# Optimization experiments

Hardware: AMD Instinct MI355X
Metric: run time of the kernel (lower is better)

Reference implementation:

```python
import jax, jax.numpy as jnp
import numpy as np

SLOPE = 0.01  # nn.LeakyReLU(negative_slope=0.01)
B, D, H, E, NH = 16384, 17, 256, 64, 4  # batch, input_dim, hidden, embed, heads

def lrelu(x):
    return jnp.where(x >= 0, x, SLOPE * x)

def setup_inputs() -> dict:
    key = jax.random.key(0)
    ks = jax.random.split(key, 16)
    s = 0.08  # ~xavier-ish scale for these widths
    return {
        "x":   jax.random.normal(ks[0], (B, D), jnp.float32),
        # per-dimension subnets, batched over the D=17 subnet axis
        "W1":  jax.random.normal(ks[1], (D, H), jnp.float32) * 1.0,      # 1 -> H
        "b1":  jnp.zeros((D, H), jnp.float32),
        "Wm":  jax.random.normal(ks[2], (2, D, H, H), jnp.float32) * s,  # two middle H->H layers
        "bm":  jnp.zeros((2, D, H), jnp.float32),
        "Wf":  jax.random.normal(ks[3], (D, H, E), jnp.float32) * s,     # H -> output_dim(=E)
        "bf":  jnp.zeros((D, E), jnp.float32),
        # MultiheadAttention in/out projections (torch Linear convention: y = x @ W.T + b)
        "Wq":  jax.random.normal(ks[4], (E, E), jnp.float32) * s,
        "bq":  jnp.zeros((E,), jnp.float32),
        "Wk":  jax.random.normal(ks[5], (E, E), jnp.float32) * s,
        "bk":  jnp.zeros((E,), jnp.float32),
        "Wv":  jax.random.normal(ks[6], (E, E), jnp.float32) * s,
        "bv":  jnp.zeros((E,), jnp.float32),
        "Wo":  jax.random.normal(ks[7], (E, E), jnp.float32) * s,
        "bo":  jnp.zeros((E,), jnp.float32),
        "Wfc": jax.random.normal(ks[8], (E, 1), jnp.float32) * s,
        "bfc": jnp.zeros((1,), jnp.float32),
    }

def reference(x, W1, b1, Wm, bm, Wf, bf, Wq, bq, Wk, bk, Wv, bv, Wo, bo, Wfc, bfc):
    b, d = x.shape
    # batched tiny subnets: first layer is (B,D,1) x (D,1,H) == outer product
    h = lrelu(x[:, :, None] * W1[None] + b1)                    # (B,D,H)
    for l in range(Wm.shape[0]):                                 # fixed 2 middle layers
        h = lrelu(jnp.einsum('bih,iho->bio', h, Wm[l]) + bm[l])  # (B,D,H)
    tokens = jnp.einsum('bih,iho->bio', h, Wf) + bf              # (B,D,E); proj is None (dims match)
    # self-attention (torch MultiheadAttention, batch_first)
    hd = E // NH
    def heads(t):
        return t.reshape(b, d, NH, hd).transpose(0, 2, 1, 3)     # (B,NH,D,hd)
    q = heads(tokens @ Wq.T + bq)
    k = heads(tokens @ Wk.T + bk)
    v = heads(tokens @ Wv.T + bv)
    scores = jnp.einsum('bhqd,bhkd->bhqk', q, k) / jnp.sqrt(jnp.asarray(hd, x.dtype))
    attn = jax.nn.softmax(scores, axis=-1)                       # (B,NH,D,D)
    o = jnp.einsum('bhqk,bhkd->bhqd', attn, v)
    o = o.transpose(0, 2, 1, 3).reshape(b, d, E) @ Wo.T + bo     # (B,D,E)
    pooled = o.mean(axis=1)                                      # (B,E)
    return lrelu(pooled @ Wfc + bfc)                             # (B,1)
```

## Files before the change

kernel.cpp:

```cpp
#include <hip/hip_runtime.h>
#include <hip/hip_bf16.h>

#define B_N   16384
#define D_N   17
#define H_N   256
#define E_N   64

typedef __attribute__((ext_vector_type(8))) short bf16x8;
typedef __attribute__((ext_vector_type(4))) float f32x4;

#define WAITV(N) asm volatile("s_waitcnt vmcnt(" #N ")" ::: "memory")
#define WAITL()  asm volatile("s_waitcnt lgkmcnt(0)" ::: "memory")
#define BAR()    __builtin_amdgcn_s_barrier()

static __device__ __forceinline__ short f2bf(float f){
  unsigned u = __builtin_bit_cast(unsigned, f);
  unsigned r = (u + 0x7fffu + ((u >> 16) & 1u)) >> 16;
  return (short)(unsigned short)r;
}
static __device__ __forceinline__ float bf2f(short s){
  unsigned u = ((unsigned)(unsigned short)s) << 16;
  return __builtin_bit_cast(float, u);
}
static __device__ __forceinline__ float lrelu(float v){ return fmaxf(v, 0.01f * v); }

static __device__ __forceinline__ void gload_lds16(const short* g, short* l){
  __builtin_amdgcn_global_load_lds(
      (const __attribute__((address_space(1))) unsigned int*)g,
      (__attribute__((address_space(3))) unsigned int*)l, 16, 0, 0);
}

__global__ void transpose_convert(const float* __restrict__ in, short* __restrict__ outp,
                                  int R, int C){
  __shared__ float tile[32][33];
  int g = blockIdx.z;
  const float* inp = in + (size_t)g * R * C;
  short* op = outp + (size_t)g * R * C;
  int c0 = blockIdx.x * 32, r0 = blockIdx.y * 32;
  for (int i = threadIdx.y; i < 32; i += 8)
    tile[i][threadIdx.x] = inp[(size_t)(r0 + i) * C + c0 + threadIdx.x];
  __syncthreads();
  for (int i = threadIdx.y; i < 32; i += 8)
    op[(size_t)(c0 + i) * R + r0 + threadIdx.x] = f2bf(tile[threadIdx.x][i]);
}

__global__ void convert_wqkv(const float* __restrict__ Wq, const float* __restrict__ Wk,
                             const float* __restrict__ Wv, short* __restrict__ outw){
  int i = blockIdx.x * 256 + threadIdx.x;
  int g = i >> 12, r = i & 4095;
  const float* W = (g == 0) ? Wq : (g == 1 ? Wk : Wv);
  outw[i] = f2bf(W[r]);
}

__global__ void wcomb_kernel(const float* __restrict__ Wo, const float* __restrict__ Wfc,
                             const float* __restrict__ bo, const float* __restrict__ bfc,
                             float* __restrict__ wcomb){
  int e = threadIdx.x;
  float acc = 0.f;
  for (int eo = 0; eo < 64; ++eo) acc += Wo[eo * 64 + e] * Wfc[eo];
  wcomb[e] = acc;
  if (e == 0){
    float bc = bfc[0];
    for (int eo = 0; eo < 64; ++eo) bc += bo[eo] * Wfc[eo];
    wcomb[64] = bc;
  }
}

static __device__ __forceinline__ void stage_w256(const short* Wt, int kk, short* wb,
                                                  int tid, int wave){
  #pragma unroll
  for (int r = 0; r < 2; ++r){
    int li = r * 512 + tid;
    int n  = li >> 2;
    int cc = (li & 3) ^ ((n >> 1) & 3);
    gload_lds16(Wt + n * 256 + kk * 32 + cc * 8,
                wb + (size_t)(r * 512 + wave * 64) * 8);
  }
}
static __device__ __forceinline__ void stage_wf_pair(const short* Wfd, int kk0, short* wb,
                                                     int tid, int wave){
  int sub = tid >> 8;
  int u   = tid & 255;
  int n   = u >> 2;
  int cc  = (u & 3) ^ ((n >> 1) & 3);
  gload_lds16(Wfd + n * 256 + (kk0 + sub) * 32 + cc * 8,
              wb + sub * 2048 + (size_t)((wave & 3) * 64) * 8);
}

__global__ __launch_bounds__(512, 2) void subnet_kernel(
    const float* __restrict__ x, const float* __restrict__ W1, const float* __restrict__ b1,
    const float* __restrict__ bm, const float* __restrict__ bf_,
    const float* __restrict__ bq, const float* __restrict__ bk, const float* __restrict__ bv,
    const short* __restrict__ WmT, const short* __restrict__ WfT, const short* __restrict__ Wqkv,
    short* __restrict__ qkv)
{
  __shared__ short hbuf[2][64 * 256];
  __shared__ short wbuf[3][256 * 32];

  int wg = blockIdx.x;
  int idx = (wg & 7) * 272 + (wg >> 3);
  const int d  = idx >> 7;
  const int m0 = (idx & 127) * 128;

  const int tid = threadIdx.x;
  const int lane = tid & 63, wave = tid >> 6;
  const int mh = wave >> 2, wv = wave & 3;
  const int l15 = lane & 15, lhi = lane >> 4;
  short* hb = &hbuf[mh][0];

  const short* WtL0 = WmT + (size_t)(0 * D_N + d) * (H_N * H_N);
  const short* WtL1 = WmT + (size_t)(1 * D_N + d) * (H_N * H_N);
  const short* Wfd  = WfT + (size_t)d * (E_N * H_N);

  stage_w256(WtL0, 0, &wbuf[0][0], tid, wave);
  stage_w256(WtL0, 1, &wbuf[1][0], tid, wave);

  {
    const int kp = tid & 127;
    const int mq = tid >> 7;
    const int tl = mq >> 1, half = mq & 1;
    short* hp = &hbuf[tl][0];
    const float w1a = W1[d * H_N + 2 * kp], w1b = W1[d * H_N + 2 * kp + 1];
    const float b1a = b1[d * H_N + 2 * kp], b1b = b1[d * H_N + 2 * kp + 1];
    #pragma unroll
    for (int i = 0; i < 32; ++i){
      int m = half * 32 + i;
      float xv = x[(size_t)(m0 + tl * 64 + m) * D_N + d];
      unsigned lo = (unsigned short)f2bf(lrelu(xv * w1a + b1a));
      unsigned hi = (unsigned short)f2bf(lrelu(xv * w1b + b1b));
      int byte = m * 512 + ((((kp >> 2) ^ (m & 7))) << 4) + ((kp & 3) << 2);
      *(unsigned*)((char*)hp + byte) = lo | (hi << 16);
    }
  }
  WAITL();

  for (int L = 0; L < 2; ++L){
    const float* bias = bm + (size_t)(L * D_N + d) * H_N;
    f32x4 acc[4][4];
    #pragma unroll
    for (int a = 0; a < 4; ++a)
      #pragma unroll
      for (int c = 0; c < 4; ++c) acc[a][c] = (f32x4){0.f, 0.f, 0.f, 0.f};

    for (int kk = 0; kk < 8; ++kk){
      const int s = L * 8 + kk;
      if (s == 15) { WAITV(1); } else { WAITV(2); }
      BAR();
      const int s2 = s + 2;
      if (s2 < 8)       stage_w256(WtL0, s2,            &wbuf[s2 % 3][0], tid, wave);
      else if (s2 < 16) stage_w256(WtL1, s2 - 8,        &wbuf[s2 % 3][0], tid, wave);
      else              stage_wf_pair(Wfd, (s2 - 16) * 2, &wbuf[s2 % 3][0], tid, wave);

      const short* wb = &wbuf[s % 3][0];
      bf16x8 af[4], bfr[4];
      #pragma unroll
      for (int fr = 0; fr < 4; ++fr){
        int row = fr * 16 + l15;
        int cch = kk * 4 + lhi;
        af[fr] = *(const bf16x8*)((const char*)hb + row * 512 + ((cch ^ (row & 7)) << 4));
      }
      #pragma unroll
      for (int fc = 0; fc < 4; ++fc){
        int n = wv * 64 + fc * 16 + l15;
        bfr[fc] = *(const bf16x8*)((const char*)wb + n * 64 + ((lhi ^ ((n >> 1) & 3)) << 4));
      }
      #pragma unroll
      for (int fr = 0; fr < 4; ++fr)
        #pragma unroll
        for (int fc = 0; fc < 4; ++fc)
          acc[fr][fc] = __builtin_amdgcn_mfma_f32_16x16x32_bf16(af[fr], bfr[fc], acc[fr][fc], 0, 0, 0);
    }
    BAR();
    #pragma unroll
    for (int fr = 0; fr < 4; ++fr)
      #pragma unroll
      for (int fc = 0; fc < 4; ++fc)
        #pragma unroll
        for (int j = 0; j < 4; ++j){
          int row = fr * 16 + lhi * 4 + j;
          int col = wv * 64 + fc * 16 + l15;
          float v = lrelu(acc[fr][fc][j] + bias[col]);
          int byte = row * 512 + ((((col >> 3) ^ (row & 7))) << 4) + ((col & 7) << 1);
          *(short*)((char*)hb + byte) = f2bf(v);
        }
    WAITL();
  }

  {
    const int r0 = wv * 16;
    f32x4 acc[4];
    #pragma unroll
    for (int fc = 0; fc < 4; ++fc) acc[fc] = (f32x4){0.f, 0.f, 0.f, 0.f};
    for (int t = 0; t < 4; ++t){
      if (t == 3) { WAITV(0); } else { WAITV(1); }
      BAR();
      if (t < 2) stage_wf_pair(Wfd, (t + 2) * 2, &wbuf[(18 + t) % 3][0], tid, wave);
      const short* wbase = &wbuf[(16 + t) % 3][0];
      #pragma unroll
      for (int kkh = 0; kkh < 2; ++kkh){
        int kk = 2 * t + kkh;
        int row = r0 + l15;
        int cch = kk * 4 + lhi;
        bf16x8 a = *(const bf16x8*)((const char*)hb + row * 512 + ((cch ^ (row & 7)) << 4));
        const short* wbs = wbase + kkh * 2048;
        #pragma unroll
        for (int fc = 0; fc < 4; ++fc){
          int n = fc * 16 + l15;
          bf16x8 b = *(const bf16x8*)((const char*)wbs + n * 64 + ((lhi ^ ((n >> 1) & 3)) << 4));
          acc[fc] = __builtin_amdgcn_mfma_f32_16x16x32_bf16(a, b, acc[fc], 0, 0, 0);
        }
      }
    }
    BAR();
    #pragma unroll
    for (int fc = 0; fc < 4; ++fc)
      #pragma unroll
      for (int j = 0; j < 4; ++j){
        int row = r0 + lhi * 4 + j;
        int col = fc * 16 + l15;
        float v = acc[fc][j] + bf_[d * E_N + col];
        int byte = row * 128 + ((((col >> 3) ^ (row & 7))) << 4) + ((col & 7) << 1);
        *(short*)((char*)hb + byte) = f2bf(v);
      }
    WAITL();
    BAR();
  }

  {
    f32x4 acc[4][3];
    #pragma unroll
    for (int fr = 0; fr < 4; ++fr)
      #pragma unroll
      for (int fc = 0; fc < 3; ++fc) acc[fr][fc] = (f32x4){0.f, 0.f, 0.f, 0.f};
    #pragma unroll
    for (int kk = 0; kk < 2; ++kk){
      bf16x8 af[4];
      #pragma unroll
      for (int fr = 0; fr < 4; ++fr){
        int row = fr * 16 + l15;
        int cch = kk * 4 + lhi;
        af[fr] = *(const bf16x8*)((const char*)hb + row * 128 + ((cch ^ (row & 7)) << 4));
      }
      bf16x8 bb[3];
      #pragma unroll
      for (int fc = 0; fc < 3; ++fc){
        int n = wv * 48 + fc * 16 + l15;
        bb[fc] = *(const bf16x8*)(Wqkv + (size_t)n * E_N + kk * 32 + lhi * 8);
      }
      #pragma unroll
      for (int fr = 0; fr < 4; ++fr)
        #pragma unroll
        for (int fc = 0; fc < 3; ++fc)
          acc[fr][fc] = __builtin_amdgcn_mfma_f32_16x16x32_bf16(af[fr], bb[fc], acc[fr][fc], 0, 0, 0);
    }
    #pragma unroll
    for (int fr = 0; fr < 4; ++fr)
      #pragma unroll
      for (int fc = 0; fc < 3; ++fc)
        #pragma unroll
        for (int j = 0; j < 4; ++j){
          int n = wv * 48 + fc * 16 + l15;
          int g = n >> 6, nl = n & 63;
          float bias = (g == 0) ? bq[nl] : (g == 1 ? bk[nl] : bv[nl]);
          int bg = m0 + mh * 64 + fr * 16 + lhi * 4 + j;
          float v = acc[fr][fc][j] + bias;
          qkv[((size_t)bg * D_N + d) * 192 + n] = f2bf(v);
        }
  }
}

__global__ __launch_bounds__(256, 2) void attn_kernel(
    const short* __restrict__ qkv, const float* __restrict__ wc, float* __restrict__ out)
{
  __shared__ short smem[4][17 * 192];
  const int tid = threadIdx.x, lane = tid & 63, wave = tid >> 6;
  const int h = lane >> 4, iq = lane & 15;

  const int b = blockIdx.x * 4 + wave;
  const short* src = qkv + (size_t)b * (17 * 192);
  for (int g0 = lane; g0 < 408; g0 += 64){
    int i = g0 / 24, c = g0 % 24;
    bf16x8 v = *(const bf16x8*)(src + g0 * 8);
    *(bf16x8*)((char*)&smem[wave][0] + i * 384 + ((c ^ (i & 7)) << 4)) = v;
  }

  float vt = 0.f, vt16 = 0.f;
  #pragma unroll
  for (int u2 = 0; u2 < 2; ++u2){
    int cch = 16 + 2 * h + u2;
    bf16x8 vj  = *(const bf16x8*)((char*)&smem[wave][0] + iq * 384 + ((cch ^ (iq & 7)) << 4));
    bf16x8 v16 = *(const bf16x8*)((char*)&smem[wave][0] + 16 * 384 + (cch << 4));
    #pragma unroll
    for (int z = 0; z < 8; ++z){
      float w = wc[h * 16 + u2 * 8 + z];
      vt   += bf2f(vj[z])  * w;
      vt16 += bf2f(v16[z]) * w;
    }
  }

  float part = 0.f;
  #pragma unroll 1
  for (int t = 0; t < 2; ++t){
    const int i = (t == 0) ? iq : 16;
    float q[16];
    #pragma unroll
    for (int u2 = 0; u2 < 2; ++u2){
      int cch = 2 * h + u2;
      bf16x8 v = *(const bf16x8*)((char*)&smem[wave][0] + i * 384 + ((cch ^ (i & 7)) << 4));
      #pragma unroll
      for (int z = 0; z < 8; ++z) q[u2 * 8 + z] = bf2f(v[z]);
    }
    float num = 0.f, den = 0.f;
    #pragma unroll 1
    for (int j = 0; j < 16; ++j){
      float a2 = 0.f;
      #pragma unroll
      for (int u2 = 0; u2 < 2; ++u2){
        int cch = 8 + 2 * h + u2;
        bf16x8 v = *(const bf16x8*)((char*)&smem[wave][0] + j * 384 + ((cch ^ (j & 7)) << 4));
        #pragma unroll
        for (int z = 0; z < 8; ++z) a2 += q[u2 * 8 + z] * bf2f(v[z]);
      }
      float e = __expf(a2 * 0.25f);
      num += e * __shfl(vt, (lane & 48) + j);
      den += e;
    }
    {
      float a2 = 0.f;
      #pragma unroll
      for (int u2 = 0; u2 < 2; ++u2){
        int cch = 8 + 2 * h + u2;
        bf16x8 v = *(const bf16x8*)((char*)&smem[wave][0] + 16 * 384 + (cch << 4));
        #pragma unroll
        for (int z = 0; z < 8; ++z) a2 += q[u2 * 8 + z] * bf2f(v[z]);
      }
      float e = __expf(a2 * 0.25f);
      num += e * vt16;
      den += e;
    }
    float contrib = num / den;
    part += (t == 0 || iq == 0) ? contrib : 0.f;
  }
  #pragma unroll
  for (int off = 1; off < 64; off <<= 1) part += __shfl_xor(part, off);
  if (lane == 0) out[b] = lrelu(part * (1.f / 17.f) + wc[64]);
}

extern "C" void kernel_launch(void* const* d_in, const int* in_sizes, int n_in,
                              void* d_out, int out_size, void* d_ws, size_t ws_size,
                              hipStream_t stream)
{
  const float* x   = (const float*)d_in[0];
  const float* W1  = (const float*)d_in[1];
  const float* b1  = (const float*)d_in[2];
  const float* Wm  = (const float*)d_in[3];
  const float* bm  = (const float*)d_in[4];
  const float* Wf  = (const float*)d_in[5];
  const float* bf_ = (const float*)d_in[6];
  const float* Wq  = (const float*)d_in[7];
  const float* bq  = (const float*)d_in[8];
  const float* Wk  = (const float*)d_in[9];
  const float* bk  = (const float*)d_in[10];
  const float* Wv  = (const float*)d_in[11];
  const float* bv  = (const float*)d_in[12];
  const float* Wo  = (const float*)d_in[13];
  const float* bo  = (const float*)d_in[14];
  const float* Wfc = (const float*)d_in[15];
  const float* bfc = (const float*)d_in[16];
  float* out = (float*)d_out;
  (void)in_sizes; (void)n_in; (void)out_size; (void)ws_size;

  char* ws = (char*)d_ws;
  size_t off = 0;
  auto alloc = [&](size_t bytes) -> char* {
    char* p = ws + off;
    off = (off + bytes + 255) & ~(size_t)255;
    return p;
  };
  short* qkvb  = (short*)alloc((size_t)B_N * D_N * 192 * 2);
  short* WmT   = (short*)alloc((size_t)2 * D_N * H_N * H_N * 2);
  short* WfT   = (short*)alloc((size_t)D_N * E_N * H_N * 2);
  short* Wqkvb = (short*)alloc((size_t)192 * E_N * 2);
  float* wcomb = (float*)alloc(65 * sizeof(float));

  transpose_convert<<<dim3(8, 8, 2 * D_N), dim3(32, 8), 0, stream>>>(Wm, WmT, 256, 256);
  transpose_convert<<<dim3(2, 8, D_N),     dim3(32, 8), 0, stream>>>(Wf, WfT, 256, 64);
  convert_wqkv<<<dim3(48), dim3(256), 0, stream>>>(Wq, Wk, Wv, Wqkvb);
  wcomb_kernel<<<dim3(1), dim3(64), 0, stream>>>(Wo, Wfc, bo, bfc, wcomb);

  subnet_kernel<<<dim3(128 * D_N), dim3(512), 0, stream>>>(
      x, W1, b1, bm, bf_, bq, bk, bv, WmT, WfT, Wqkvb, qkvb);

  attn_kernel<<<dim3(4096), dim3(256), 0, stream>>>(qkvb, wcomb, out);
}
```

Baseline: 244.1 us.

## Halve subnet tile to 64 rows per block to raise occupancy

Each subnet workgroup now processes 64 batch rows instead of 128, with one shared activation buffer. Waves are split 2x4 over rows and columns, and the final-projection and QKV stages are remapped so all 8 waves share the work. This cuts accumulator registers and LDS per block, allowing 4 blocks per CU instead of 2 and doubling the grid. In exchange, each block re-stages the full per-dimension weights for half as many rows, so weight traffic and staging overhead per output row double.

Result: faster. 230.2 us (median of 2 runs) (-5.7%).

```diff
diff --git a/kernel.cpp b/kernel.cpp
--- a/kernel.cpp
+++ b/kernel.cpp
@@ -87,26 +87,25 @@
               wb + sub * 2048 + (size_t)((wave & 3) * 64) * 8);
 }
 
-__global__ __launch_bounds__(512, 2) void subnet_kernel(
+__global__ __launch_bounds__(512, 4) void subnet_kernel(
     const float* __restrict__ x, const float* __restrict__ W1, const float* __restrict__ b1,
     const float* __restrict__ bm, const float* __restrict__ bf_,
     const float* __restrict__ bq, const float* __restrict__ bk, const float* __restrict__ bv,
     const short* __restrict__ WmT, const short* __restrict__ WfT, const short* __restrict__ Wqkv,
     short* __restrict__ qkv)
 {
-  __shared__ short hbuf[2][64 * 256];
+  __shared__ short hbuf[64 * 256];
   __shared__ short wbuf[3][256 * 32];
 
   int wg = blockIdx.x;
-  int idx = (wg & 7) * 272 + (wg >> 3);
-  const int d  = idx >> 7;
-  const int m0 = (idx & 127) * 128;
+  int idx = (wg & 7) * 544 + (wg >> 3);
+  const int d  = idx >> 8;
+  const int m0 = (idx & 255) * 64;
 
   const int tid = threadIdx.x;
   const int lane = tid & 63, wave = tid >> 6;
-  const int mh = wave >> 2, wv = wave & 3;
+  const int wr = wave >> 2, wv = wave & 3;
   const int l15 = lane & 15, lhi = lane >> 4;
-  short* hb = &hbuf[mh][0];
 
   const short* WtL0 = WmT + (size_t)(0 * D_N + d) * (H_N * H_N);
   const short* WtL1 = WmT + (size_t)(1 * D_N + d) * (H_N * H_N);
@@ -118,27 +117,25 @@
   {
     const int kp = tid & 127;
     const int mq = tid >> 7;
-    const int tl = mq >> 1, half = mq & 1;
-    short* hp = &hbuf[tl][0];
     const float w1a = W1[d * H_N + 2 * kp], w1b = W1[d * H_N + 2 * kp + 1];
     const float b1a = b1[d * H_N + 2 * kp], b1b = b1[d * H_N + 2 * kp + 1];
     #pragma unroll
-    for (int i = 0; i < 32; ++i){
-      int m = half * 32 + i;
-      float xv = x[(size_t)(m0 + tl * 64 + m) * D_N + d];
+    for (int i = 0; i < 16; ++i){
+      int m = mq * 16 + i;
+      float xv = x[(size_t)(m0 + m) * D_N + d];
       unsigned lo = (unsigned short)f2bf(lrelu(xv * w1a + b1a));
       unsigned hi = (unsigned short)f2bf(lrelu(xv * w1b + b1b));
       int byte = m * 512 + ((((kp >> 2) ^ (m & 7))) << 4) + ((kp & 3) << 2);
-      *(unsigned*)((char*)hp + byte) = lo | (hi << 16);
+      *(unsigned*)((char*)&hbuf[0] + byte) = lo | (hi << 16);
     }
   }
   WAITL();
 
   for (int L = 0; L < 2; ++L){
     const float* bias = bm + (size_t)(L * D_N + d) * H_N;
-    f32x4 acc[4][4];
-    #pragma unroll
-    for (int a = 0; a < 4; ++a)
+    f32x4 acc[2][4];
+    #pragma unroll
+    for (int a = 0; a < 2; ++a)
       #pragma unroll
       for (int c = 0; c < 4; ++c) acc[a][c] = (f32x4){0.f, 0.f, 0.f, 0.f};
 
@@ -147,17 +144,17 @@
       if (s == 15) { WAITV(1); } else { WAITV(2); }
       BAR();
       const int s2 = s + 2;
-      if (s2 < 8)       stage_w256(WtL0, s2,            &wbuf[s2 % 3][0], tid, wave);
-      else if (s2 < 16) stage_w256(WtL1, s2 - 8,        &wbuf[s2 % 3][0], tid, wave);
+      if (s2 < 8)       stage_w256(WtL0, s2,              &wbuf[s2 % 3][0], tid, wave);
+      else if (s2 < 16) stage_w256(WtL1, s2 - 8,          &wbuf[s2 % 3][0], tid, wave);
       else              stage_wf_pair(Wfd, (s2 - 16) * 2, &wbuf[s2 % 3][0], tid, wave);
 
       const short* wb = &wbuf[s % 3][0];
-      bf16x8 af[4], bfr[4];
-      #pragma unroll
-      for (int fr = 0; fr < 4; ++fr){
-        int row = fr * 16 + l15;
+      bf16x8 af[2], bfr[4];
+      #pragma unroll
+      for (int fr = 0; fr < 2; ++fr){
+        int row = wr * 32 + fr * 16 + l15;
         int cch = kk * 4 + lhi;
-        af[fr] = *(const bf16x8*)((const char*)hb + row * 512 + ((cch ^ (row & 7)) << 4));
+        af[fr] = *(const bf16x8*)((const char*)&hbuf[0] + row * 512 + ((cch ^ (row & 7)) << 4));
       }
       #pragma unroll
       for (int fc = 0; fc < 4; ++fc){
@@ -165,32 +162,32 @@
         bfr[fc] = *(const bf16x8*)((const char*)wb + n * 64 + ((lhi ^ ((n >> 1) & 3)) << 4));
       }
       #pragma unroll
-      for (int fr = 0; fr < 4; ++fr)
+      for (int fr = 0; fr < 2; ++fr)
         #pragma unroll
         for (int fc = 0; fc < 4; ++fc)
           acc[fr][fc] = __builtin_amdgcn_mfma_f32_16x16x32_bf16(af[fr], bfr[fc], acc[fr][fc], 0, 0, 0);
     }
     BAR();
     #pragma unroll
-    for (int fr = 0; fr < 4; ++fr)
+    for (int fr = 0; fr < 2; ++fr)
       #pragma unroll
       for (int fc = 0; fc < 4; ++fc)
         #pragma unroll
         for (int j = 0; j < 4; ++j){
-          int row = fr * 16 + lhi * 4 + j;
+          int row = wr * 32 + fr * 16 + lhi * 4 + j;
           int col = wv * 64 + fc * 16 + l15;
           float v = lrelu(acc[fr][fc][j] + bias[col]);
           int byte = row * 512 + ((((col >> 3) ^ (row & 7))) << 4) + ((col & 7) << 1);
-          *(short*)((char*)hb + byte) = f2bf(v);
+          *(short*)((char*)&hbuf[0] + byte) = f2bf(v);
         }
     WAITL();
   }
 
   {
-    const int r0 = wv * 16;
-    f32x4 acc[4];
-    #pragma unroll
-    for (int fc = 0; fc < 4; ++fc) acc[fc] = (f32x4){0.f, 0.f, 0.f, 0.f};
+    const int r0 = (wave >> 1) * 16, c0 = (wave & 1) * 32;
+    f32x4 acc[2];
+    acc[0] = (f32x4){0.f, 0.f, 0.f, 0.f};
+    acc[1] = (f32x4){0.f, 0.f, 0.f, 0.f};
     for (int t = 0; t < 4; ++t){
       if (t == 3) { WAITV(0); } else { WAITV(1); }
       BAR();
@@ -201,11 +198,11 @@
         int kk = 2 * t + kkh;
         int row = r0 + l15;
         int cch = kk * 4 + lhi;
-        bf16x8 a = *(const bf16x8*)((const char*)hb + row * 512 + ((cch ^ (row & 7)) << 4));
+        bf16x8 a = *(const bf16x8*)((const char*)&hbuf[0] + row * 512 + ((cch ^ (row & 7)) << 4));
         const short* wbs = wbase + kkh * 2048;
         #pragma unroll
-        for (int fc = 0; fc < 4; ++fc){
-          int n = fc * 16 + l15;
+        for (int fc = 0; fc < 2; ++fc){
+          int n = c0 + fc * 16 + l15;
           bf16x8 b = *(const bf16x8*)((const char*)wbs + n * 64 + ((lhi ^ ((n >> 1) & 3)) << 4));
           acc[fc] = __builtin_amdgcn_mfma_f32_16x16x32_bf16(a, b, acc[fc], 0, 0, 0);
         }
@@ -213,59 +210,47 @@
     }
     BAR();
     #pragma unroll
-    for (int fc = 0; fc < 4; ++fc)
+    for (int fc = 0; fc < 2; ++fc)
       #pragma unroll
       for (int j = 0; j < 4; ++j){
         int row = r0 + lhi * 4 + j;
-        int col = fc * 16 + l15;
+        int col = c0 + fc * 16 + l15;
         float v = acc[fc][j] + bf_[d * E_N + col];
         int byte = row * 128 + ((((col >> 3) ^ (row & 7))) << 4) + ((col & 7) << 1);
-        *(short*)((char*)hb + byte) = f2bf(v);
+        *(short*)((char*)&hbuf[0] + byte) = f2bf(v);
       }
     WAITL();
     BAR();
   }
 
   {
-    f32x4 acc[4][3];
-    #pragma unroll
-    for (int fr = 0; fr < 4; ++fr)
-      #pragma unroll
-      for (int fc = 0; fc < 3; ++fc) acc[fr][fc] = (f32x4){0.f, 0.f, 0.f, 0.f};
+    const int r0 = (wave & 3) * 16, c0 = (wave >> 2) * 96;
+    f32x4 acc[6];
+    #pragma unroll
+    for (int fc = 0; fc < 6; ++fc) acc[fc] = (f32x4){0.f, 0.f, 0.f, 0.f};
     #pragma unroll
     for (int kk = 0; kk < 2; ++kk){
-      bf16x8 af[4];
-      #pragma unroll
-      for (int fr = 0; fr < 4; ++fr){
-        int row = fr * 16 + l15;
-        int cch = kk * 4 + lhi;
-        af[fr] = *(const bf16x8*)((const char*)hb + row * 128 + ((cch ^ (row & 7)) << 4));
-      }
-      bf16x8 bb[3];
-      #pragma unroll
-      for (int fc = 0; fc < 3; ++fc){
-        int n = wv * 48 + fc * 16 + l15;
-        bb[fc] = *(const bf16x8*)(Wqkv + (size_t)n * E_N + kk * 32 + lhi * 8);
-      }
-      #pragma unroll
-      for (int fr = 0; fr < 4; ++fr)
-        #pragma unroll
-        for (int fc = 0; fc < 3; ++fc)
-          acc[fr][fc] = __builtin_amdgcn_mfma_f32_16x16x32_bf16(af[fr], bb[fc], acc[fr][fc], 0, 0, 0);
-    }
-    #pragma unroll
-    for (int fr = 0; fr < 4; ++fr)
-      #pragma unroll
-      for (int fc = 0; fc < 3; ++fc)
-        #pragma unroll
-        for (int j = 0; j < 4; ++j){
-          int n = wv * 48 + fc * 16 + l15;
-          int g = n >> 6, nl = n & 63;
-          float bias = (g == 0) ? bq[nl] : (g == 1 ? bk[nl] : bv[nl]);
-          int bg = m0 + mh * 64 + fr * 16 + lhi * 4 + j;
-          float v = acc[fr][fc][j] + bias;
-          qkv[((size_t)bg * D_N + d) * 192 + n] = f2bf(v);
-        }
+      int row = r0 + l15;
+      int cch = kk * 4 + lhi;
+      bf16x8 a = *(const bf16x8*)((const char*)&hbuf[0] + row * 128 + ((cch ^ (row & 7)) << 4));
+      #pragma unroll
+      for (int fc = 0; fc < 6; ++fc){
+        int n = c0 + fc * 16 + l15;
+        bf16x8 b = *(const bf16x8*)(Wqkv + (size_t)n * E_N + kk * 32 + lhi * 8);
+        acc[fc] = __builtin_amdgcn_mfma_f32_16x16x32_bf16(a, b, acc[fc], 0, 0, 0);
+      }
+    }
+    #pragma unroll
+    for (int fc = 0; fc < 6; ++fc)
+      #pragma unroll
+      for (int j = 0; j < 4; ++j){
+        int n = c0 + fc * 16 + l15;
+        int g = n >> 6, nl = n & 63;
+        float bias = (g == 0) ? bq[nl] : (g == 1 ? bk[nl] : bv[nl]);
+        int bg = m0 + r0 + lhi * 4 + j;
+        float v = acc[fc][j] + bias;
+        qkv[((size_t)bg * D_N + d) * 192 + n] = f2bf(v);
+      }
   }
 }
 
@@ -388,7 +373,7 @@
   convert_wqkv<<<dim3(48), dim3(256), 0, stream>>>(Wq, Wk, Wv, Wqkvb);
   wcomb_kernel<<<dim3(1), dim3(64), 0, stream>>>(Wo, Wfc, bo, bfc, wcomb);
 
-  subnet_kernel<<<dim3(128 * D_N), dim3(512), 0, stream>>>(
+  subnet_kernel<<<dim3(256 * D_N), dim3(512), 0, stream>>>(
       x, W1, b1, bm, bf_, bq, bk, bv, WmT, WfT, Wqkvb, qkvb);
 
   attn_kernel<<<dim3(4096), dim3(256), 0, stream>>>(qkvb, wcomb, out);
```
